# Kernel tuning notes

Measured on AMD Instinct MI355X. Metric: run time of the kernel, lower is better.

The kernel has to match this reference:

```python
import jax, jax.numpy as jnp
import numpy as np

HID = 256      # hard-coded hidden_size in the torch module
LEVELS = 16    # topological levels in the generated DAG


def _lstm_cell(x, h, c, Wih, Whh, bih, bhh):
    # PyTorch LSTM cell: gates ordered (input, forget, cell, output)
    g = x @ Wih.T + h @ Whh.T + bih + bhh
    i, f, gg, o = jnp.split(g, 4, axis=-1)
    c_new = jax.nn.sigmoid(f) * c + jax.nn.sigmoid(i) * jnp.tanh(gg)
    h_new = jax.nn.sigmoid(o) * jnp.tanh(c_new)
    return h_new, c_new


def _forward(tokens, parents_idx, parent_valid,
             Wih_tok, Whh_tok, bih_tok, bhh_tok,
             Wih_ins, Whh_ins, bih_ins, bhh_ins, Wlin, blin):
    N, T, E = tokens.shape
    K = N // LEVELS
    NEG = jnp.asarray(-1e30, tokens.dtype)

    # --- token-level LSTM over each instruction's tokens, batched across instrs ---
    def tok_step(carry, x):
        h, c = carry
        return _lstm_cell(x, h, c, Wih_tok, Whh_tok, bih_tok, bhh_tok), None
    z = jnp.zeros((N, HID), tokens.dtype)
    (ins_embed, _), _ = jax.lax.scan(tok_step, (z, z), tokens.transpose(1, 0, 2))
    # ins_embed: [N, HID] = final token-LSTM hidden per instruction

    # --- instruction-level LSTM over the DAG, level by level ---
    H = jnp.zeros((N, HID), tokens.dtype)
    C = jnp.zeros((N, HID), tokens.dtype)
    for l in range(LEVELS):
        sl = slice(l * K, (l + 1) * K)
        pidx = parents_idx[sl]                 # [K, P] indices into earlier levels
        pval = parent_valid[sl][..., None]     # [K, P, 1]
        ph = jnp.where(pval, H[pidx], NEG).max(axis=1)   # max-reduction combine
        pc = jnp.where(pval, C[pidx], NEG).max(axis=1)
        has = parent_valid[sl].any(axis=1, keepdims=True)
        h0 = jnp.where(has, ph, 0.0)           # no parents -> zero init_hidden
        c0 = jnp.where(has, pc, 0.0)
        h1, c1 = _lstm_cell(ins_embed[sl], h0, c0, Wih_ins, Whh_ins, bih_ins, bhh_ins)
        H = H.at[sl].set(h1)
        C = C.at[sl].set(c1)

    # roots = instructions with no children (never referenced as a parent)
    appears = jnp.zeros((N,), jnp.int32).at[parents_idx.reshape(-1)].add(
        parent_valid.reshape(-1).astype(jnp.int32))
    root = (appears == 0)[:, None]
    final = jnp.where(root, H, NEG).max(axis=0)   # [HID]
    return final @ Wlin.T + blin                   # [num_classes]


def setup_inputs() -> dict:
    N, T, E, P = 2048, 16, 512, 8
    K = N // LEVELS
    rng = np.random.default_rng(0)
    pidx = np.zeros((N, P), np.int32)
    pval = np.zeros((N, P), bool)
    for l in range(1, LEVELS):
        pidx[l * K:(l + 1) * K] = rng.integers(0, l * K, (K, P))
        pval[l * K:(l + 1) * K] = rng.random((K, P)) < 0.75
    key = jax.random.key(0)
    ks = jax.random.split(key, 6)
    s = lambda k, shape, fan: jax.random.normal(k, shape, jnp.float32) / np.float32(np.sqrt(fan))
    return {
        "tokens": jax.random.normal(ks[0], (N, T, E), jnp.float32),
        "parents_idx": jnp.asarray(pidx),
        "parent_valid": jnp.asarray(pval),
        "Wih_tok": s(ks[1], (4 * HID, E), E),
        "Whh_tok": s(ks[2], (4 * HID, HID), HID),
        "bih_tok": jnp.zeros((4 * HID,), jnp.float32),
        "bhh_tok": jnp.zeros((4 * HID,), jnp.float32),
        "Wih_ins": s(ks[3], (4 * HID, HID), HID),
        "Whh_ins": s(ks[4], (4 * HID, HID), HID),
        "bih_ins": jnp.zeros((4 * HID,), jnp.float32),
        "bhh_ins": jnp.zeros((4 * HID,), jnp.float32),
        "Wlin": s(ks[5], (1, HID), HID),
        "blin": jnp.zeros((1,), jnp.float32),
    }


def reference(tokens, parents_idx, parent_valid,
              Wih_tok, Whh_tok, bih_tok, bhh_tok,
              Wih_ins, Whh_ins, bih_ins, bhh_ins, Wlin, blin):
    return _forward(tokens, parents_idx, parent_valid,
                    Wih_tok, Whh_tok, bih_tok, bhh_tok,
                    Wih_ins, Whh_ins, bih_ins, bhh_ins, Wlin, blin)
```

## Files before the change

kernel.cpp:

```cpp
#include <hip/hip_runtime.h>

#define NTOK 2048
#define TT   16
#define EE   512
#define HIDD 256
#define G4   1024
#define NLVL 16
#define KLVL 128
#define INV2048 (1.0f/2048.0f)

typedef _Float16 v8h __attribute__((ext_vector_type(8)));
typedef _Float16 v4h __attribute__((ext_vector_type(4)));
typedef float    v4f __attribute__((ext_vector_type(4)));

__device__ __forceinline__ v4f mfma16(v8h a, v8h b, v4f c) {
  return __builtin_amdgcn_mfma_f32_16x16x32_f16(a, b, c, 0, 0, 0);
}

__device__ __forceinline__ float fsig(float x) {
  return 1.0f / (1.0f + __expf(-x));
}
__device__ __forceinline__ float ftanh(float x) {
  float ax = fabsf(x);
  float e  = __expf(-2.0f * ax);
  float t  = (1.0f - e) / (1.0f + e);
  return copysignf(t, x);
}

__device__ __forceinline__ void split8(const v4f& w0, const v4f& w1, v8h& hi, v8h& lo) {
#pragma unroll
  for (int u = 0; u < 4; ++u) {
    float v = w0[u]; _Float16 h = (_Float16)v;
    hi[u] = h; lo[u] = (_Float16)((v - (float)h) * 2048.0f);
  }
#pragma unroll
  for (int u = 0; u < 4; ++u) {
    float v = w1[u]; _Float16 h = (_Float16)v;
    hi[4+u] = h; lo[4+u] = (_Float16)((v - (float)h) * 2048.0f);
  }
}

__device__ __forceinline__ v8h cvt8(const v4f& w0, const v4f& w1) {
  v8h r;
#pragma unroll
  for (int u = 0; u < 4; ++u) { r[u] = (_Float16)w0[u]; r[4+u] = (_Float16)w1[u]; }
  return r;
}

__global__ __launch_bounds__(256) void knorm(const void* __restrict__ pv_raw,
                                             unsigned char* __restrict__ pv8) {
  __shared__ int mode;
  const int tid = threadIdx.x;
  if (tid == 0) mode = 0;
  __syncthreads();
  const unsigned* pu = (const unsigned*)pv_raw;
  int local = 0;
  for (int i = tid; i < 4096; i += 256) {
    unsigned v = pu[i];
    if (v == 0x3F800000u) { local = 2; break; }
    if (v > 1u) local = 1;
  }
  if (local) atomicMax(&mode, local);
  __syncthreads();
  const int m = mode;
  const unsigned char* pb = (const unsigned char*)pv_raw;
  const float* pf = (const float*)pv_raw;
  const int* pi = (const int*)pv_raw;
  for (int i = tid; i < NTOK * 8; i += 256) {
    unsigned char v;
    if (m == 1)      v = (pb[i] != 0);
    else if (m == 2) v = (pf[i] != 0.0f);
    else             v = (pi[i] != 0);
    pv8[i] = v;
  }
}

__global__ __launch_bounds__(256) void kw_cvt(
    const float* __restrict__ a0, _Float16* __restrict__ f0,
    const float* __restrict__ a1, _Float16* __restrict__ f1,
    const float* __restrict__ a2, _Float16* __restrict__ f2,
    const float* __restrict__ a3, _Float16* __restrict__ f3) {
  int i = blockIdx.x * 256 + threadIdx.x;
  if (blockIdx.x < 1024) {
    const int row = i >> 8, col = i & 255;
    const int fc = row >> 4, l15 = row & 15;
    const int kk = col >> 5, lq = (col >> 3) & 3, u = col & 7;
    const int lane8 = (lq * 16 + l15) * 8 + u;
    float v; _Float16 h;
    v = a0[i]; f0[(size_t)(fc * 8 + kk) * 512 + lane8] = (_Float16)v;
    const size_t base = (size_t)(fc * 8 + kk) * 1024 + lane8;
    v = a1[i]; h = (_Float16)v; f1[base] = h; f1[base + 512] = (_Float16)((v - (float)h) * 2048.0f);
    v = a2[i]; h = (_Float16)v; f2[base] = h; f2[base + 512] = (_Float16)((v - (float)h) * 2048.0f);
  } else {
    int k = i - 262144;
    const int row = k >> 9, col = k & 511;
    const int fc = row >> 4, l15 = row & 15;
    const int kk = col >> 5, lq = (col >> 3) & 3, u = col & 7;
    f3[(size_t)(fc * 16 + kk) * 512 + (lq * 16 + l15) * 8 + u] = (_Float16)a3[k];
  }
}

__global__ __launch_bounds__(512, 1) void kg2(const float* __restrict__ A,
                                              const _Float16* __restrict__ WtH,
                                              const float* __restrict__ b1,
                                              const float* __restrict__ b2,
                                              _Float16* __restrict__ Xg, int h) {
  __shared__ _Float16 As[64 * 520];
  const int tid  = threadIdx.x;
  const int lane = tid & 63;
  const int nq   = tid >> 6;
  const int l15  = lane & 15;
  const int lq   = lane >> 4;
  const int m0   = blockIdx.x * 64;

#pragma unroll
  for (int p = 0; p < 4; ++p) {
    const int row  = p * 16 + (tid >> 5);
    const int col0 = (tid & 31) * 16;
    const int ar   = m0 + row;
    const int tokrow = (ar & 2047) * 16 + h * 8 + (ar >> 11);
    const float* s = A + (size_t)tokrow * EE + col0;
    v4f x0 = *(const v4f*)s, x1 = *(const v4f*)(s + 4);
    v4f x2 = *(const v4f*)(s + 8), x3 = *(const v4f*)(s + 12);
    _Float16* d = As + row * 520 + col0;
    *(v8h*)d       = cvt8(x0, x1);
    *(v8h*)(d + 8) = cvt8(x2, x3);
  }
  __syncthreads();

  v4f acc[4][8];
#pragma unroll
  for (int n = 0; n < 8; ++n) {
    const int col = (nq * 8 + n) * 16 + l15;
    const float bb = b1[col] + b2[col];
#pragma unroll
    for (int m = 0; m < 4; ++m) acc[m][n] = (v4f){bb, bb, bb, bb};
  }

#pragma unroll 4
  for (int kk = 0; kk < 16; ++kk) {
    v8h af[4];
#pragma unroll
    for (int m = 0; m < 4; ++m)
      af[m] = *(const v8h*)(As + (m * 16 + l15) * 520 + kk * 32 + lq * 8);
#pragma unroll
    for (int n = 0; n < 8; ++n) {
      const int fc = nq * 8 + n;
      v8h bh = *(const v8h*)(WtH + (size_t)(fc * 16 + kk) * 512 + lane * 8);
#pragma unroll
      for (int m = 0; m < 4; ++m) acc[m][n] = mfma16(af[m], bh, acc[m][n]);
    }
  }

#pragma unroll
  for (int m = 0; m < 4; ++m)
#pragma unroll
    for (int n = 0; n < 8; ++n) {
      const int row = m0 + m * 16 + lq * 4;
      const int col = (nq * 8 + n) * 16 + l15;
      v4h o;
#pragma unroll
      for (int r = 0; r < 4; ++r) o[r] = (_Float16)acc[m][n][r];
      *(v4h*)(Xg + ((size_t)(row >> 2) * G4 + col) * 4) = o;
    }
}

__global__ __launch_bounds__(512, 1) void kr2(const _Float16* __restrict__ Xg,
                                              const _Float16* __restrict__ WhhH,
                                              float* __restrict__ Hst,
                                              float* __restrict__ Cst,
                                              float* __restrict__ emb, int q) {
  __shared__ float hbuf[16 * 260];
  const int tid  = threadIdx.x;
  const int lane = tid & 63;
  const int w    = tid >> 6;
  const int wv   = w & 3;
  const int jh   = w >> 2;
  const int l15  = lane & 15;
  const int lq   = lane >> 4;
  const int r0   = blockIdx.x * 16;

  v4f c[2];
  if (q) {
#pragma unroll
    for (int j2 = 0; j2 < 2; ++j2) {
      const int feat = 16 * (wv + 4 * (2 * jh + j2)) + l15;
#pragma unroll
      for (int r = 0; r < 4; ++r)
        c[j2][r] = Cst[(size_t)(r0 + lq * 4 + r) * HIDD + feat];
    }
    for (int idx = tid; idx < 4096; idx += 512)
      hbuf[(idx >> 8) * 260 + (idx & 255)] = Hst[(size_t)(r0 + (idx >> 8)) * HIDD + (idx & 255)];
  } else {
    c[0] = (v4f){0.f, 0.f, 0.f, 0.f};
    c[1] = (v4f){0.f, 0.f, 0.f, 0.f};
  }
  __syncthreads();

  v4h xp[4][2];
  {
    const size_t xrow = (size_t)((r0 >> 2) + lq) * G4;
#pragma unroll
    for (int g = 0; g < 4; ++g)
#pragma unroll
      for (int j2 = 0; j2 < 2; ++j2) {
        const int col = 256 * g + 16 * (wv + 4 * (2 * jh + j2)) + l15;
        xp[g][j2] = *(const v4h*)(Xg + (xrow + col) * 4);
      }
  }

#pragma unroll 1
  for (int tl = 0; tl < 8; ++tl) {
    const bool have_h = (q > 0) || (tl > 0);
    v4f acc[4][2];
#pragma unroll
    for (int g = 0; g < 4; ++g)
#pragma unroll
      for (int j2 = 0; j2 < 2; ++j2) {
        v4f a;
#pragma unroll
        for (int r = 0; r < 4; ++r) a[r] = (float)xp[g][j2][r];
        acc[g][j2] = a;
      }
    if (tl < 7) {
      const size_t xrow = (size_t)((tl + 1) * 512 + (r0 >> 2) + lq) * G4;
#pragma unroll
      for (int g = 0; g < 4; ++g)
#pragma unroll
        for (int j2 = 0; j2 < 2; ++j2) {
          const int col = 256 * g + 16 * (wv + 4 * (2 * jh + j2)) + l15;
          xp[g][j2] = *(const v4h*)(Xg + (xrow + col) * 4);
        }
    }
    if (have_h) {
#pragma unroll
      for (int kk = 0; kk < 8; ++kk) {
        const int ko = kk * 32 + lq * 8;
        v4f w0 = *(const v4f*)(hbuf + l15 * 260 + ko);
        v4f w1 = *(const v4f*)(hbuf + l15 * 260 + ko + 4);
        v8h ah = cvt8(w0, w1);
#pragma unroll
        for (int g = 0; g < 4; ++g)
#pragma unroll
          for (int j2 = 0; j2 < 2; ++j2) {
            const int fc = 16 * g + wv + 4 * (2 * jh + j2);
            acc[g][j2] = mfma16(ah,
                *(const v8h*)(WhhH + (size_t)(fc * 8 + kk) * 512 + lane * 8),
                acc[g][j2]);
          }
      }
    }
    __syncthreads();
#pragma unroll
    for (int j2 = 0; j2 < 2; ++j2) {
      const int feat = 16 * (wv + 4 * (2 * jh + j2)) + l15;
#pragma unroll
      for (int r = 0; r < 4; ++r) {
        const int rr = lq * 4 + r;
        float cn = fsig(acc[1][j2][r]) * c[j2][r] + fsig(acc[0][j2][r]) * ftanh(acc[2][j2][r]);
        float hn = fsig(acc[3][j2][r]) * ftanh(cn);
        c[j2][r] = cn;
        hbuf[rr * 260 + feat] = hn;
        if (tl == 7) {
          const size_t grow = r0 + rr;
          if (!q) { Hst[grow * HIDD + feat] = hn; Cst[grow * HIDD + feat] = cn; }
          else    { emb[grow * HIDD + feat] = hn; }
        }
      }
    }
    __syncthreads();
  }
}

__global__ __launch_bounds__(256) void kapp(const int* __restrict__ pidx,
                                            const unsigned char* __restrict__ pval,
                                            int* __restrict__ appears) {
  int e = blockIdx.x * 512 + threadIdx.x * 2;
#pragma unroll
  for (int u = 0; u < 2; ++u, ++e) {
    if (pval[e]) atomicAdd(appears + pidx[e], 1);
  }
}

__global__ __launch_bounds__(256) void klevel(
    const float* __restrict__ emb,
    const _Float16* __restrict__ WihF, const _Float16* __restrict__ WhhF,
    const float* __restrict__ bi, const float* __restrict__ bh,
    const int* __restrict__ pidx, const unsigned char* __restrict__ pval,
    float* __restrict__ H, float* __restrict__ C, int l) {
  __shared__ float h0s[16 * 260];
  __shared__ float c0s[16 * 260];
  __shared__ int      pis[128];
  __shared__ unsigned char pvs[128];
  const int tid  = threadIdx.x;
  const int lane = tid & 63;
  const int wv   = tid >> 6;
  const int l15  = lane & 15;
  const int lq   = lane >> 4;
  const int b    = blockIdx.x;
  const int mf   = b >> 2;
  const int q    = b & 3;
  const int fi   = q * 4 + wv;

  if (tid < 128) {
    int rr = tid >> 3, p = tid & 7;
    int row = l * KLVL + mf * 16 + rr;
    pis[tid] = pidx[row * 8 + p];
    pvs[tid] = pval[row * 8 + p];
  }
  __syncthreads();
#pragma unroll 1
  for (int it = 0; it < 4; ++it) {
    int task = tid + 256 * it;
    int rr = task >> 6;
    int f4 = (task & 63) * 4;
    v4f hm = (v4f){-1e30f, -1e30f, -1e30f, -1e30f};
    v4f cm = hm;
    bool any = false;
#pragma unroll
    for (int p = 0; p < 8; ++p) {
      if (pvs[rr * 8 + p]) {
        any = true;
        int par = pis[rr * 8 + p];
        v4f hv = *(const v4f*)(H + (size_t)par * HIDD + f4);
        v4f cv = *(const v4f*)(C + (size_t)par * HIDD + f4);
#pragma unroll
        for (int u = 0; u < 4; ++u) { hm[u] = fmaxf(hm[u], hv[u]); cm[u] = fmaxf(cm[u], cv[u]); }
      }
    }
    if (!any) { hm = (v4f){0.f,0.f,0.f,0.f}; cm = (v4f){0.f,0.f,0.f,0.f}; }
    *(v4f*)(h0s + rr * 260 + f4) = hm;
    *(v4f*)(c0s + rr * 260 + f4) = cm;
  }
  __syncthreads();

  v4f acc1[4], acc2[4];
#pragma unroll
  for (int g = 0; g < 4; ++g) {
    int col  = 256 * g + 16 * fi + l15;
    float bb = bi[col] + bh[col];
    acc1[g] = (v4f){bb, bb, bb, bb};
    acc2[g] = (v4f){0.f, 0.f, 0.f, 0.f};
  }
  const int arow = l * KLVL + mf * 16 + l15;
#pragma unroll 1
  for (int kk = 0; kk < 8; ++kk) {
    const int ko = kk * 32 + lq * 8;
    v4f x0 = *(const v4f*)(emb + (size_t)arow * HIDD + ko);
    v4f x1 = *(const v4f*)(emb + (size_t)arow * HIDD + ko + 4);
    v8h axh, axl;
    split8(x0, x1, axh, axl);
#pragma unroll
    for (int g = 0; g < 4; ++g) {
      const int fc = 16 * g + fi;
      const _Float16* p = WihF + (size_t)(fc * 8 + kk) * 1024 + lane * 8;
      v8h bh8 = *(const v8h*)p;
      v8h bl8 = *(const v8h*)(p + 512);
      acc1[g] = mfma16(axh, bh8, acc1[g]);
      acc2[g] = mfma16(axl, bh8, acc2[g]);
      acc2[g] = mfma16(axh, bl8, acc2[g]);
    }
  }
#pragma unroll 1
  for (int kk = 0; kk < 8; ++kk) {
    const int ko = kk * 32 + lq * 8;
    v4f h0 = *(const v4f*)(h0s + l15 * 260 + ko);
    v4f h1 = *(const v4f*)(h0s + l15 * 260 + ko + 4);
    v8h ahh, ahl;
    split8(h0, h1, ahh, ahl);
#pragma unroll
    for (int g = 0; g < 4; ++g) {
      const int fc = 16 * g + fi;
      const _Float16* p = WhhF + (size_t)(fc * 8 + kk) * 1024 + lane * 8;
      v8h bh8 = *(const v8h*)p;
      v8h bl8 = *(const v8h*)(p + 512);
      acc1[g] = mfma16(ahh, bh8, acc1[g]);
      acc2[g] = mfma16(ahl, bh8, acc2[g]);
      acc2[g] = mfma16(ahh, bl8, acc2[g]);
    }
  }
#pragma unroll
  for (int r = 0; r < 4; ++r) {
    int rr = lq * 4 + r;
    int n  = 16 * fi + l15;
    float ig = acc1[0][r] + acc2[0][r] * INV2048;
    float fg = acc1[1][r] + acc2[1][r] * INV2048;
    float gg = acc1[2][r] + acc2[2][r] * INV2048;
    float og = acc1[3][r] + acc2[3][r] * INV2048;
    float c0 = c0s[rr * 260 + n];
    float cn = fsig(fg) * c0 + fsig(ig) * ftanh(gg);
    float hn = fsig(og) * ftanh(cn);
    int grow = l * KLVL + mf * 16 + rr;
    H[(size_t)grow * HIDD + n] = hn;
    C[(size_t)grow * HIDD + n] = cn;
  }
}

__global__ __launch_bounds__(256) void kroot1(const float* __restrict__ H,
                                              const int* __restrict__ appears,
                                              float* __restrict__ pmax) {
  __shared__ int app[64];
  const int tid = threadIdx.x;
  const int rb  = blockIdx.x * 64;
  if (tid < 64) app[tid] = appears[rb + tid];
  __syncthreads();
  float m = -1e30f;
#pragma unroll 1
  for (int r = 0; r < 64; ++r) {
    if (app[r] == 0) m = fmaxf(m, H[(size_t)(rb + r) * HIDD + tid]);
  }
  pmax[blockIdx.x * 256 + tid] = m;
}

__global__ __launch_bounds__(256) void kroot2(const float* __restrict__ pmax,
                                              const float* __restrict__ Wlin,
                                              const float* __restrict__ blin,
                                              float* __restrict__ out) {
  __shared__ float red[256];
  const int tid = threadIdx.x;
  float m = pmax[tid];
#pragma unroll 1
  for (int bb = 1; bb < 32; ++bb) m = fmaxf(m, pmax[bb * 256 + tid]);
  red[tid] = m * Wlin[tid];
  __syncthreads();
  if (tid == 0) {
    float s = 0.f;
    for (int i2 = 0; i2 < 256; ++i2) s += red[i2];
    out[0] = s + blin[0];
  }
}

extern "C" void kernel_launch(void* const* d_in, const int* in_sizes, int n_in,
                              void* d_out, int out_size, void* d_ws, size_t ws_size,
                              hipStream_t stream) {
  const float* tokens  = (const float*)d_in[0];
  const int*   pidx    = (const int*)d_in[1];
  const void*  pvraw   = (const void*)d_in[2];
  const float* Wih_tok = (const float*)d_in[3];
  const float* Whh_tok = (const float*)d_in[4];
  const float* bih_tok = (const float*)d_in[5];
  const float* bhh_tok = (const float*)d_in[6];
  const float* Wih_ins = (const float*)d_in[7];
  const float* Whh_ins = (const float*)d_in[8];
  const float* bih_ins = (const float*)d_in[9];
  const float* bhh_ins = (const float*)d_in[10];
  const float* Wlin    = (const float*)d_in[11];
  const float* blin    = (const float*)d_in[12];

  char* ws = (char*)d_ws;
  const size_t OFF_XG    = 0;
  const size_t OFF_H     = OFF_XG   + 33554432;
  const size_t OFF_C     = OFF_H    + 2097152;
  const size_t OFF_EMB   = OFF_C    + 2097152;
  const size_t OFF_WHHT  = OFF_EMB  + 2097152;
  const size_t OFF_WIHIF = OFF_WHHT + 524288;
  const size_t OFF_WHHIF = OFF_WIHIF + 1048576;
  const size_t OFF_WTH   = OFF_WHHIF + 1048576;
  const size_t OFF_APP   = OFF_WTH  + 1048576;
  const size_t OFF_PMX   = OFF_APP  + 8192;
  const size_t OFF_PV8   = OFF_PMX  + 32768;

  _Float16* Xg    = (_Float16*)(ws + OFF_XG);
  float*    Hbuf  = (float*)(ws + OFF_H);
  float*    Cbuf  = (float*)(ws + OFF_C);
  float*    emb   = (float*)(ws + OFF_EMB);
  _Float16* WhhT  = (_Float16*)(ws + OFF_WHHT);
  _Float16* WihIF = (_Float16*)(ws + OFF_WIHIF);
  _Float16* WhhIF = (_Float16*)(ws + OFF_WHHIF);
  _Float16* WtH   = (_Float16*)(ws + OFF_WTH);
  int*      app   = (int*)(ws + OFF_APP);
  float*    pmx   = (float*)(ws + OFF_PMX);
  unsigned char* pv8 = (unsigned char*)(ws + OFF_PV8);

  hipMemsetAsync(ws + OFF_APP, 0, 8192, stream);

  knorm<<<dim3(1), dim3(256), 0, stream>>>(pvraw, pv8);
  kw_cvt<<<dim3(3072), dim3(256), 0, stream>>>(Whh_tok, WhhT,
                                               Wih_ins, WihIF,
                                               Whh_ins, WhhIF,
                                               Wih_tok, WtH);
  kapp<<<dim3(32), dim3(256), 0, stream>>>(pidx, pv8, app);

  for (int h = 0; h < 2; ++h) {
    kg2<<<dim3(256), dim3(512), 0, stream>>>(tokens, WtH, bih_tok, bhh_tok, Xg, h);
    kr2<<<dim3(128), dim3(512), 0, stream>>>(Xg, WhhT, Hbuf, Cbuf, emb, h);
  }

  for (int l = 0; l < NLVL; ++l) {
    klevel<<<dim3(32), dim3(256), 0, stream>>>(emb, WihIF, WhhIF,
                                               bih_ins, bhh_ins, pidx, pv8,
                                               Hbuf, Cbuf, l);
  }
  kroot1<<<dim3(32), dim3(256), 0, stream>>>(Hbuf, app, pmx);
  kroot2<<<dim3(1), dim3(256), 0, stream>>>(pmx, Wlin, blin, (float*)d_out);
}
```

Measured before the change: 611.3 us.

## Vectorize weight conversion, double-buffer recurrent kernel, drop split-fp16 in level LSTM

Several changes land together. The weight conversion kernel now has each thread handle eight contiguous floats with vector loads and stores. The token recurrence kernel double-buffers its shared hidden state, removing one barrier per step, and software-prefetches recurrent weight fragments into registers. The level kernel stores the instruction embedding in fp16 and drops the hi/lo split-precision MFMAs in favour of single fp16 products, which cuts MFMA count and memory traffic but loses accuracy compared with the compensated scheme. The level kernel also splits the parent max-reduction for h and c across different thread mappings.

Measured after the change: 576.1 us. 1.06x faster.

```diff
diff --git a/kernel.cpp b/kernel.cpp
--- a/kernel.cpp
+++ b/kernel.cpp
@@ -80,23 +80,37 @@
     const float* __restrict__ a1, _Float16* __restrict__ f1,
     const float* __restrict__ a2, _Float16* __restrict__ f2,
     const float* __restrict__ a3, _Float16* __restrict__ f3) {
-  int i = blockIdx.x * 256 + threadIdx.x;
-  if (blockIdx.x < 1024) {
-    const int row = i >> 8, col = i & 255;
+  const int t = blockIdx.x * 256 + threadIdx.x;
+  if (t < 32768) {
+    const int row = t >> 5, col8 = (t & 31) * 8;
     const int fc = row >> 4, l15 = row & 15;
-    const int kk = col >> 5, lq = (col >> 3) & 3, u = col & 7;
-    const int lane8 = (lq * 16 + l15) * 8 + u;
-    float v; _Float16 h;
-    v = a0[i]; f0[(size_t)(fc * 8 + kk) * 512 + lane8] = (_Float16)v;
-    const size_t base = (size_t)(fc * 8 + kk) * 1024 + lane8;
-    v = a1[i]; h = (_Float16)v; f1[base] = h; f1[base + 512] = (_Float16)((v - (float)h) * 2048.0f);
-    v = a2[i]; h = (_Float16)v; f2[base] = h; f2[base + 512] = (_Float16)((v - (float)h) * 2048.0f);
+    const int kk = col8 >> 5, lq = (col8 >> 3) & 3;
+    const int lane8 = (lq * 16 + l15) * 8;
+    const size_t srow = (size_t)row * 256 + col8;
+    {
+      v4f x0 = *(const v4f*)(a0 + srow), x1 = *(const v4f*)(a0 + srow + 4);
+      *(v8h*)(f0 + (size_t)(fc * 8 + kk) * 512 + lane8) = cvt8(x0, x1);
+    }
+    {
+      v4f x0 = *(const v4f*)(a1 + srow), x1 = *(const v4f*)(a1 + srow + 4);
+      v8h hi, lo; split8(x0, x1, hi, lo);
+      _Float16* d = f1 + (size_t)(fc * 8 + kk) * 1024 + lane8;
+      *(v8h*)d = hi; *(v8h*)(d + 512) = lo;
+    }
+    {
+      v4f x0 = *(const v4f*)(a2 + srow), x1 = *(const v4f*)(a2 + srow + 4);
+      v8h hi, lo; split8(x0, x1, hi, lo);
+      _Float16* d = f2 + (size_t)(fc * 8 + kk) * 1024 + lane8;
+      *(v8h*)d = hi; *(v8h*)(d + 512) = lo;
+    }
   } else {
-    int k = i - 262144;
-    const int row = k >> 9, col = k & 511;
+    const int k = t - 32768;
+    const int row = k >> 6, col8 = (k & 63) * 8;
     const int fc = row >> 4, l15 = row & 15;
-    const int kk = col >> 5, lq = (col >> 3) & 3, u = col & 7;
-    f3[(size_t)(fc * 16 + kk) * 512 + (lq * 16 + l15) * 8 + u] = (_Float16)a3[k];
+    const int kk = col8 >> 5, lq = (col8 >> 3) & 3;
+    const size_t srow = (size_t)row * 512 + col8;
+    v4f x0 = *(const v4f*)(a3 + srow), x1 = *(const v4f*)(a3 + srow + 4);
+    *(v8h*)(f3 + (size_t)(fc * 16 + kk) * 512 + (lq * 16 + l15) * 8) = cvt8(x0, x1);
   }
 }
 
@@ -165,12 +179,12 @@
     }
 }
 
-__global__ __launch_bounds__(512, 1) void kr2(const _Float16* __restrict__ Xg,
+__global__ __launch_bounds__(512, 1) void kr3(const _Float16* __restrict__ Xg,
                                               const _Float16* __restrict__ WhhH,
                                               float* __restrict__ Hst,
                                               float* __restrict__ Cst,
-                                              float* __restrict__ emb, int q) {
-  __shared__ float hbuf[16 * 260];
+                                              _Float16* __restrict__ emb, int q) {
+  __shared__ float hbuf[2][16 * 260];
   const int tid  = threadIdx.x;
   const int lane = tid & 63;
   const int w    = tid >> 6;
@@ -180,6 +194,8 @@
   const int lq   = lane >> 4;
   const int r0   = blockIdx.x * 16;
 
+  const _Float16* wbase = WhhH + (size_t)(8 * jh + wv) * 4096 + lane * 8;
+
   v4f c[2];
   if (q) {
 #pragma unroll
@@ -190,12 +206,11 @@
         c[j2][r] = Cst[(size_t)(r0 + lq * 4 + r) * HIDD + feat];
     }
     for (int idx = tid; idx < 4096; idx += 512)
-      hbuf[(idx >> 8) * 260 + (idx & 255)] = Hst[(size_t)(r0 + (idx >> 8)) * HIDD + (idx & 255)];
+      hbuf[0][(idx >> 8) * 260 + (idx & 255)] = Hst[(size_t)(r0 + (idx >> 8)) * HIDD + (idx & 255)];
   } else {
     c[0] = (v4f){0.f, 0.f, 0.f, 0.f};
     c[1] = (v4f){0.f, 0.f, 0.f, 0.f};
   }
-  __syncthreads();
 
   v4h xp[4][2];
   {
@@ -209,8 +224,17 @@
       }
   }
 
+  v8h bA[8], bB[8];
+#pragma unroll
+  for (int g = 0; g < 4; ++g)
+#pragma unroll
+    for (int j2 = 0; j2 < 2; ++j2)
+      bA[g * 2 + j2] = *(const v8h*)(wbase + (16 * g + 4 * j2) * 4096);
+  __syncthreads();
+
 #pragma unroll 1
   for (int tl = 0; tl < 8; ++tl) {
+    const int cur = tl & 1;
     const bool have_h = (q > 0) || (tl > 0);
     v4f acc[4][2];
 #pragma unroll
@@ -234,23 +258,51 @@
     }
     if (have_h) {
 #pragma unroll
-      for (int kk = 0; kk < 8; ++kk) {
-        const int ko = kk * 32 + lq * 8;
-        v4f w0 = *(const v4f*)(hbuf + l15 * 260 + ko);
-        v4f w1 = *(const v4f*)(hbuf + l15 * 260 + ko + 4);
-        v8h ah = cvt8(w0, w1);
+      for (int kp = 0; kp < 4; ++kp) {
+        const int k0 = 2 * kp, k1 = 2 * kp + 1;
 #pragma unroll
         for (int g = 0; g < 4; ++g)
 #pragma unroll
-          for (int j2 = 0; j2 < 2; ++j2) {
-            const int fc = 16 * g + wv + 4 * (2 * jh + j2);
-            acc[g][j2] = mfma16(ah,
-                *(const v8h*)(WhhH + (size_t)(fc * 8 + kk) * 512 + lane * 8),
-                acc[g][j2]);
-          }
-      }
-    }
-    __syncthreads();
+          for (int j2 = 0; j2 < 2; ++j2)
+            bB[g * 2 + j2] = *(const v8h*)(wbase + (16 * g + 4 * j2) * 4096 + k1 * 512);
+        {
+          const int ko = k0 * 32 + lq * 8;
+          v4f w0 = *(const v4f*)(hbuf[cur] + l15 * 260 + ko);
+          v4f w1 = *(const v4f*)(hbuf[cur] + l15 * 260 + ko + 4);
+          v8h ah = cvt8(w0, w1);
+#pragma unroll
+          for (int g = 0; g < 4; ++g)
+#pragma unroll
+            for (int j2 = 0; j2 < 2; ++j2)
+              acc[g][j2] = mfma16(ah, bA[g * 2 + j2], acc[g][j2]);
+        }
+        if (kp < 3) {
+#pragma unroll
+          for (int g = 0; g < 4; ++g)
+#pragma unroll
+            for (int j2 = 0; j2 < 2; ++j2)
+              bA[g * 2 + j2] = *(const v8h*)(wbase + (16 * g + 4 * j2) * 4096 + (k1 + 1) * 512);
+        }
+        {
+          const int ko = k1 * 32 + lq * 8;
+          v4f w0 = *(const v4f*)(hbuf[cur] + l15 * 260 + ko);
+          v4f w1 = *(const v4f*)(hbuf[cur] + l15 * 260 + ko + 4);
+          v8h ah = cvt8(w0, w1);
+#pragma unroll
+          for (int g = 0; g < 4; ++g)
+#pragma unroll
+            for (int j2 = 0; j2 < 2; ++j2)
+              acc[g][j2] = mfma16(ah, bB[g * 2 + j2], acc[g][j2]);
+        }
+      }
+      if (tl < 7) {
+#pragma unroll
+        for (int g = 0; g < 4; ++g)
+#pragma unroll
+          for (int j2 = 0; j2 < 2; ++j2)
+            bA[g * 2 + j2] = *(const v8h*)(wbase + (16 * g + 4 * j2) * 4096);
+      }
+    }
 #pragma unroll
     for (int j2 = 0; j2 < 2; ++j2) {
       const int feat = 16 * (wv + 4 * (2 * jh + j2)) + l15;
@@ -260,11 +312,11 @@
         float cn = fsig(acc[1][j2][r]) * c[j2][r] + fsig(acc[0][j2][r]) * ftanh(acc[2][j2][r]);
         float hn = fsig(acc[3][j2][r]) * ftanh(cn);
         c[j2][r] = cn;
-        hbuf[rr * 260 + feat] = hn;
+        hbuf[cur ^ 1][rr * 260 + feat] = hn;
         if (tl == 7) {
           const size_t grow = r0 + rr;
           if (!q) { Hst[grow * HIDD + feat] = hn; Cst[grow * HIDD + feat] = cn; }
-          else    { emb[grow * HIDD + feat] = hn; }
+          else    { emb[grow * HIDD + feat] = (_Float16)hn; }
         }
       }
     }
@@ -283,13 +335,13 @@
 }
 
 __global__ __launch_bounds__(256) void klevel(
-    const float* __restrict__ emb,
+    const _Float16* __restrict__ emb,
     const _Float16* __restrict__ WihF, const _Float16* __restrict__ WhhF,
     const float* __restrict__ bi, const float* __restrict__ bh,
     const int* __restrict__ pidx, const unsigned char* __restrict__ pval,
     float* __restrict__ H, float* __restrict__ C, int l) {
-  __shared__ float h0s[16 * 260];
-  __shared__ float c0s[16 * 260];
+  __shared__ _Float16 h0s[16 * 264];
+  __shared__ float    c0s[16 * 68];
   __shared__ int      pis[128];
   __shared__ unsigned char pvs[128];
   const int tid  = threadIdx.x;
@@ -315,81 +367,69 @@
     int rr = task >> 6;
     int f4 = (task & 63) * 4;
     v4f hm = (v4f){-1e30f, -1e30f, -1e30f, -1e30f};
-    v4f cm = hm;
     bool any = false;
 #pragma unroll
     for (int p = 0; p < 8; ++p) {
       if (pvs[rr * 8 + p]) {
         any = true;
-        int par = pis[rr * 8 + p];
-        v4f hv = *(const v4f*)(H + (size_t)par * HIDD + f4);
-        v4f cv = *(const v4f*)(C + (size_t)par * HIDD + f4);
-#pragma unroll
-        for (int u = 0; u < 4; ++u) { hm[u] = fmaxf(hm[u], hv[u]); cm[u] = fmaxf(cm[u], cv[u]); }
-      }
-    }
-    if (!any) { hm = (v4f){0.f,0.f,0.f,0.f}; cm = (v4f){0.f,0.f,0.f,0.f}; }
-    *(v4f*)(h0s + rr * 260 + f4) = hm;
-    *(v4f*)(c0s + rr * 260 + f4) = cm;
-  }
-  __syncthreads();
-
-  v4f acc1[4], acc2[4];
+        v4f hv = *(const v4f*)(H + (size_t)pis[rr * 8 + p] * HIDD + f4);
+#pragma unroll
+        for (int u = 0; u < 4; ++u) hm[u] = fmaxf(hm[u], hv[u]);
+      }
+    }
+    if (!any) hm = (v4f){0.f, 0.f, 0.f, 0.f};
+    v4h h4;
+#pragma unroll
+    for (int u = 0; u < 4; ++u) h4[u] = (_Float16)hm[u];
+    *(v4h*)(h0s + rr * 264 + f4) = h4;
+  }
+  {
+    int rr = tid >> 4;
+    int cc = (tid & 15) * 4;
+    int f4 = q * 64 + cc;
+    v4f cm = (v4f){-1e30f, -1e30f, -1e30f, -1e30f};
+    bool any = false;
+#pragma unroll
+    for (int p = 0; p < 8; ++p) {
+      if (pvs[rr * 8 + p]) {
+        any = true;
+        v4f cv = *(const v4f*)(C + (size_t)pis[rr * 8 + p] * HIDD + f4);
+#pragma unroll
+        for (int u = 0; u < 4; ++u) cm[u] = fmaxf(cm[u], cv[u]);
+      }
+    }
+    if (!any) cm = (v4f){0.f, 0.f, 0.f, 0.f};
+    *(v4f*)(c0s + rr * 68 + cc) = cm;
+  }
+  __syncthreads();
+
+  v4f acc[4];
 #pragma unroll
   for (int g = 0; g < 4; ++g) {
     int col  = 256 * g + 16 * fi + l15;
     float bb = bi[col] + bh[col];
-    acc1[g] = (v4f){bb, bb, bb, bb};
-    acc2[g] = (v4f){0.f, 0.f, 0.f, 0.f};
+    acc[g] = (v4f){bb, bb, bb, bb};
   }
   const int arow = l * KLVL + mf * 16 + l15;
 #pragma unroll 1
   for (int kk = 0; kk < 8; ++kk) {
     const int ko = kk * 32 + lq * 8;
-    v4f x0 = *(const v4f*)(emb + (size_t)arow * HIDD + ko);
-    v4f x1 = *(const v4f*)(emb + (size_t)arow * HIDD + ko + 4);
-    v8h axh, axl;
-    split8(x0, x1, axh, axl);
+    v8h ax = *(const v8h*)(emb + (size_t)arow * HIDD + ko);
+    v8h ah = *(const v8h*)(h0s + l15 * 264 + ko);
 #pragma unroll
     for (int g = 0; g < 4; ++g) {
       const int fc = 16 * g + fi;
-      const _Float16* p = WihF + (size_t)(fc * 8 + kk) * 1024 + lane * 8;
-      v8h bh8 = *(const v8h*)p;
-      v8h bl8 = *(const v8h*)(p + 512);
-      acc1[g] = mfma16(axh, bh8, acc1[g]);
-      acc2[g] = mfma16(axl, bh8, acc2[g]);
-      acc2[g] = mfma16(axh, bl8, acc2[g]);
-    }
-  }
-#pragma unroll 1
-  for (int kk = 0; kk < 8; ++kk) {
-    const int ko = kk * 32 + lq * 8;
-    v4f h0 = *(const v4f*)(h0s + l15 * 260 + ko);
-    v4f h1 = *(const v4f*)(h0s + l15 * 260 + ko + 4);
-    v8h ahh, ahl;
-    split8(h0, h1, ahh, ahl);
-#pragma unroll
-    for (int g = 0; g < 4; ++g) {
-      const int fc = 16 * g + fi;
-      const _Float16* p = WhhF + (size_t)(fc * 8 + kk) * 1024 + lane * 8;
-      v8h bh8 = *(const v8h*)p;
-      v8h bl8 = *(const v8h*)(p + 512);
-      acc1[g] = mfma16(ahh, bh8, acc1[g]);
-      acc2[g] = mfma16(ahl, bh8, acc2[g]);
-      acc2[g] = mfma16(ahh, bl8, acc2[g]);
+      acc[g] = mfma16(ax, *(const v8h*)(WihF + (size_t)(fc * 8 + kk) * 1024 + lane * 8), acc[g]);
+      acc[g] = mfma16(ah, *(const v8h*)(WhhF + (size_t)(fc * 8 + kk) * 1024 + lane * 8), acc[g]);
     }
   }
 #pragma unroll
   for (int r = 0; r < 4; ++r) {
     int rr = lq * 4 + r;
     int n  = 16 * fi + l15;
-    float ig = acc1[0][r] + acc2[0][r] * INV2048;
-    float fg = acc1[1][r] + acc2[1][r] * INV2048;
-    float gg = acc1[2][r] + acc2[2][r] * INV2048;
-    float og = acc1[3][r] + acc2[3][r] * INV2048;
-    float c0 = c0s[rr * 260 + n];
-    float cn = fsig(fg) * c0 + fsig(ig) * ftanh(gg);
-    float hn = fsig(og) * ftanh(cn);
+    float c0 = c0s[rr * 68 + 16 * wv + l15];
+    float cn = fsig(acc[1][r]) * c0 + fsig(acc[0][r]) * ftanh(acc[2][r]);
+    float hn = fsig(acc[3][r]) * ftanh(cn);
     int grow = l * KLVL + mf * 16 + rr;
     H[(size_t)grow * HIDD + n] = hn;
     C[(size_t)grow * HIDD + n] = cn;
@@ -452,7 +492,7 @@
   const size_t OFF_H     = OFF_XG   + 33554432;
   const size_t OFF_C     = OFF_H    + 2097152;
   const size_t OFF_EMB   = OFF_C    + 2097152;
-  const size_t OFF_WHHT  = OFF_EMB  + 2097152;
+  const size_t OFF_WHHT  = OFF_EMB  + 1048576;
   const size_t OFF_WIHIF = OFF_WHHT + 524288;
   const size_t OFF_WHHIF = OFF_WIHIF + 1048576;
   const size_t OFF_WTH   = OFF_WHHIF + 1048576;
@@ -463,7 +503,7 @@
   _Float16* Xg    = (_Float16*)(ws + OFF_XG);
   float*    Hbuf  = (float*)(ws + OFF_H);
   float*    Cbuf  = (float*)(ws + OFF_C);
-  float*    emb   = (float*)(ws + OFF_EMB);
+  _Float16* emb   = (_Float16*)(ws + OFF_EMB);
   _Float16* WhhT  = (_Float16*)(ws + OFF_WHHT);
   _Float16* WihIF = (_Float16*)(ws + OFF_WIHIF);
   _Float16* WhhIF = (_Float16*)(ws + OFF_WHHIF);
@@ -475,15 +515,15 @@
   hipMemsetAsync(ws + OFF_APP, 0, 8192, stream);
 
   knorm<<<dim3(1), dim3(256), 0, stream>>>(pvraw, pv8);
-  kw_cvt<<<dim3(3072), dim3(256), 0, stream>>>(Whh_tok, WhhT,
-                                               Wih_ins, WihIF,
-                                               Whh_ins, WhhIF,
-                                               Wih_tok, WtH);
+  kw_cvt<<<dim3(384), dim3(256), 0, stream>>>(Whh_tok, WhhT,
+                                              Wih_ins, WihIF,
+                                              Whh_ins, WhhIF,
+                                              Wih_tok, WtH);
   kapp<<<dim3(32), dim3(256), 0, stream>>>(pidx, pv8, app);
 
   for (int h = 0; h < 2; ++h) {
     kg2<<<dim3(256), dim3(512), 0, stream>>>(tokens, WtH, bih_tok, bhh_tok, Xg, h);
-    kr2<<<dim3(128), dim3(512), 0, stream>>>(Xg, WhhT, Hbuf, Cbuf, emb, h);
+    kr3<<<dim3(128), dim3(512), 0, stream>>>(Xg, WhhT, Hbuf, Cbuf, emb, h);
   }
 
   for (int l = 0; l < NLVL; ++l) {
```
